# Performance work log

Hardware: AMD Instinct MI355X
Metric: run time of the kernel (lower is better)

The kernel has to match this reference:

```python
import jax, jax.numpy as jnp
import numpy as np
import math

B = 2048
NOSC = 64            # oscillators per modality
M = 3                # modalities (audio, text, vision) in sorted order
BDIM = 256           # binding_dim
DT = 0.01
NSTEPS = 10
DIMS = [512, 768, 1024]  # audio, text, vision
TWO_PI = 2.0 * math.pi


def setup_inputs() -> dict:
    key = jax.random.key(0)
    ks = iter(jax.random.split(key, 40))
    d = {}
    names = ['a', 't', 'v']
    for name, dim, x_key in zip(names, DIMS, ['x_audio', 'x_text', 'x_vision']):
        d[x_key] = jax.random.normal(next(ks), (B, dim), dtype=jnp.float32)
        s = 1.0 / math.sqrt(dim)
        d[f'Wf_{name}'] = jax.random.uniform(next(ks), (BDIM, dim), jnp.float32, -s, s)
        d[f'bf_{name}'] = jax.random.uniform(next(ks), (BDIM,), jnp.float32, -s, s)
        d[f'Wp_{name}'] = jax.random.uniform(next(ks), (NOSC, dim), jnp.float32, -s, s)
        d[f'bp_{name}'] = jax.random.uniform(next(ks), (NOSC,), jnp.float32, -s, s)
    # omegas: randn*0.1 + 1.0 + i*0.5 for i-th sorted modality
    for i, name in enumerate(names):
        d[f'omega_{name}'] = jax.random.normal(next(ks), (NOSC,), jnp.float32) * 0.1 + 1.0 + i * 0.5
    N = M * NOSC
    d['inter_coupling'] = jax.random.normal(next(ks), (N, N), jnp.float32) * 0.1
    s = 1.0 / math.sqrt(BDIM * M)
    d['W_fusion'] = jax.random.uniform(next(ks), (BDIM, BDIM * M), jnp.float32, -s, s)
    d['b_fusion'] = jax.random.uniform(next(ks), (BDIM,), jnp.float32, -s, s)
    return d


def reference(x_audio, x_text, x_vision,
              Wf_a, bf_a, Wp_a, bp_a,
              Wf_t, bf_t, Wp_t, bp_t,
              Wf_v, bf_v, Wp_v, bp_v,
              omega_a, omega_t, omega_v,
              inter_coupling, W_fusion, b_fusion):
    def enc(x, Wf, bf, Wp, bp):
        encoded = x @ Wf.T + bf                       # (B, BDIM)
        phases = (x @ Wp.T + bp) % TWO_PI             # (B, NOSC)
        return encoded, phases

    e_a, p_a = enc(x_audio, Wf_a, bf_a, Wp_a, bp_a)
    e_t, p_t = enc(x_text, Wf_t, bf_t, Wp_t, bp_t)
    e_v, p_v = enc(x_vision, Wf_v, bf_v, Wp_v, bp_v)

    phases = jnp.concatenate([p_a, p_t, p_v], axis=-1)        # (B, N)
    omega = jnp.concatenate([omega_a, omega_t, omega_v])      # (N,)
    K = (inter_coupling + inter_coupling.T) * 0.5             # (N, N)
    N = phases.shape[-1]

    def step(ph, _):
        diff = ph[:, :, None] - ph[:, None, :]                # (B, N, N)
        forces = jnp.einsum('ij,bij->bi', K, jnp.sin(diff)) / N
        ph = (ph + DT * (omega[None, :] + forces)) % TWO_PI
        return ph, None

    phases, _ = jax.lax.scan(step, phases, None, length=NSTEPS)

    pm = [phases[:, i * NOSC:(i + 1) * NOSC] for i in range(M)]  # per-modality

    # PLV between banks a,b: |mean_{i,j} exp(i(a_i - b_j))| = R_a * R_b where
    # R = |mean_k exp(i phi_k)| (resultant length), computed with real math.
    R = jnp.stack([jnp.sqrt(jnp.mean(jnp.cos(p), -1) ** 2 +
                            jnp.mean(jnp.sin(p), -1) ** 2) for p in pm])  # (M, B)
    bm = jnp.mean(R[:, None, :] * R[None, :, :], axis=-1)      # (M, M)
    binding_matrix = jnp.where(jnp.eye(M, dtype=bool), 1.0, bm)

    fused_parts = []
    for e, p in zip([e_a, e_t, e_v], pm):
        phase_mod = jnp.mean(jnp.cos(p), axis=-1, keepdims=True)  # (B, 1)
        fused_parts.append(e * (0.5 + 0.5 * phase_mod))
    fused = jnp.concatenate(fused_parts, axis=-1)              # (B, M*BDIM)
    bound = fused @ W_fusion.T + b_fusion                      # (B, BDIM)

    triu = jnp.triu(jnp.ones((M, M), dtype=bool), k=1)
    total = jnp.sum(jnp.where(triu, binding_matrix, 0.0)) / triu.sum()
    total_binding = jnp.full((bound.shape[0],), total)

    return bound, binding_matrix, phases, total_binding
```

## Files before the change

kernel.cpp:

```cpp
#include <hip/hip_runtime.h>
#include <math.h>

typedef short bf16x8 __attribute__((ext_vector_type(8)));
typedef short bf16x4 __attribute__((ext_vector_type(4)));
typedef float f32x4  __attribute__((ext_vector_type(4)));

#define INV_2PI  0.15915494309189535f
#define TWO_PI_F 6.283185307179586f
#define FSCALE   8.2893199e-06f

static __device__ inline short f2bf(float f) {
    union { float f; unsigned u; } v; v.f = f;
    unsigned r = (v.u + 0x7FFFu + ((v.u >> 16) & 1u)) >> 16;
    return (short)r;
}
static __device__ inline float bf2f(short h) {
    union { unsigned u; float f; } v; v.u = ((unsigned)(unsigned short)h) << 16;
    return v.f;
}

__global__ __launch_bounds__(256) void front_kernel(
    const float* __restrict__ xa, const float* __restrict__ xt, const float* __restrict__ xv,
    const float* __restrict__ Wpa, const float* __restrict__ Wpt, const float* __restrict__ Wpv,
    const float* __restrict__ IC,
    const float* __restrict__ oa, const float* __restrict__ ot, const float* __restrict__ ov,
    const float* __restrict__ bpa, const float* __restrict__ bpt, const float* __restrict__ bpv,
    float* __restrict__ partial, short* __restrict__ XB, short* __restrict__ Kp,
    float* __restrict__ om_eff, float* __restrict__ bp_all, float* __restrict__ bacc)
{
    __shared__ alignas(16) float As[16][72];
    __shared__ alignas(16) float Bs[16][72];
    int b = blockIdx.x;
    int t = threadIdx.x;

    if (b < 576) {
        int slot = b % 18, rb = b / 18;
        int z = slot < 4 ? 0 : (slot < 10 ? 1 : 2);
        int chunk = slot - (z == 0 ? 0 : (z == 1 ? 4 : 10));
        const float* A = z == 0 ? xa : (z == 1 ? xt : xv);
        const float* W = z == 0 ? Wpa : (z == 1 ? Wpt : Wpv);
        int K = z == 0 ? 512 : (z == 1 ? 768 : 1024);
        int kb = chunk * 128;
        int m0 = rb * 64;

        int tx = t & 15, ty = t >> 4;
        int row = t >> 2, c4 = t & 3;

        float acc[4][4] = {};
        float4 ar = *(const float4*)&A[(size_t)(m0 + row) * K + kb + c4 * 4];
        float4 br = *(const float4*)&W[(size_t)row * K + kb + c4 * 4];

        for (int k0 = 0; k0 < 128; k0 += 16) {
            if (k0) __syncthreads();
            As[c4 * 4 + 0][row] = ar.x;
            As[c4 * 4 + 1][row] = ar.y;
            As[c4 * 4 + 2][row] = ar.z;
            As[c4 * 4 + 3][row] = ar.w;
            Bs[c4 * 4 + 0][row] = br.x;
            Bs[c4 * 4 + 1][row] = br.y;
            Bs[c4 * 4 + 2][row] = br.z;
            Bs[c4 * 4 + 3][row] = br.w;
            __syncthreads();
            if (k0 + 16 < 128) {
                ar = *(const float4*)&A[(size_t)(m0 + row) * K + kb + k0 + 16 + c4 * 4];
                br = *(const float4*)&W[(size_t)row * K + kb + k0 + 16 + c4 * 4];
            }
#pragma unroll
            for (int kk = 0; kk < 16; ++kk) {
                float4 aq = *(const float4*)&As[kk][ty * 4];
                float4 bq = *(const float4*)&Bs[kk][tx * 4];
                float av[4] = {aq.x, aq.y, aq.z, aq.w};
                float bv[4] = {bq.x, bq.y, bq.z, bq.w};
#pragma unroll
                for (int i = 0; i < 4; ++i)
#pragma unroll
                    for (int j = 0; j < 4; ++j)
                        acc[i][j] += av[i] * bv[j];
            }
        }

        float* P = partial + (size_t)slot * 131072;
#pragma unroll
        for (int i = 0; i < 4; ++i) {
            float4 v = make_float4(acc[i][0], acc[i][1], acc[i][2], acc[i][3]);
            *(float4*)&P[(size_t)(m0 + ty * 4 + i) * 64 + tx * 4] = v;
        }
    } else if (b < 648) {
        for (int u = (b - 576) * 256 + t; u < 1179648; u += 72 * 256) {
            const float4* sp;
            if (u < 262144)      sp = (const float4*)xa + u;
            else if (u < 655360) sp = (const float4*)xt + (u - 262144);
            else                 sp = (const float4*)xv + (u - 655360);
            float4 v = *sp;
            bf16x4 h; h[0] = f2bf(v.x); h[1] = f2bf(v.y); h[2] = f2bf(v.z); h[3] = f2bf(v.w);
            *(bf16x4*)(XB + (size_t)u * 4) = h;
        }
    } else if (b < 680) {
        for (int idx = (b - 648) * 256 + t; idx < 36864; idx += 32 * 256) {
            int k = idx / 192, n = idx - k * 192;
            float v = 0.5f * (IC[k * 192 + n] + IC[n * 192 + k]);
            int nt = n >> 4, kc = k >> 5;
            int lane = ((k >> 3) & 3) * 16 + (n & 15);
            int j = k & 7;
            Kp[((nt * 6 + kc) * 64 + lane) * 8 + j] = f2bf(v);
        }
    } else {
        if (t < 192) {
            float w = t < 64 ? oa[t] : (t < 128 ? ot[t - 64] : ov[t - 128]);
            om_eff[t] = w * (0.01f * INV_2PI);
            float bb = t < 64 ? bpa[t] : (t < 128 ? bpt[t - 64] : bpv[t - 128]);
            bp_all[t] = bb;
        }
        if (t < 4) bacc[t] = 0.f;
    }
}

__global__ __launch_bounds__(256) void mid_kernel(
    const short* __restrict__ XB,
    const float* __restrict__ Wfa, const float* __restrict__ Wft, const float* __restrict__ Wfv,
    const float* __restrict__ ba, const float* __restrict__ bt, const float* __restrict__ bv,
    const float* __restrict__ partial, const float* __restrict__ bp_all,
    const short* __restrict__ Kp, const float* __restrict__ om_eff,
    short* __restrict__ e_bf16,
    float* __restrict__ phases_out, float* __restrict__ pm, float* __restrict__ bacc)
{
    __shared__ alignas(16) char smem[26816];
    int b = blockIdx.x;
    int t = threadIdx.x;
    int lane = t & 63, w = t >> 6;
    int q = lane >> 4, col = lane & 15;

    if (b < 384) {
        int z = b / 128, r = b % 128;
        int m0 = (r >> 2) * 64, n0 = (r & 3) * 64;
        const short* A    = XB + (z == 0 ? 0 : (z == 1 ? 1048576 : 2621440));
        const float* W    = z == 0 ? Wfa : (z == 1 ? Wft : Wfv);
        const float* bias = z == 0 ? ba : (z == 1 ? bt : bv);
        int K             = z == 0 ? 512 : (z == 1 ? 768 : 1024);

        short* As = (short*)smem;
        short* Bs = (short*)smem + 64 * 72;

        f32x4 acc[4];
#pragma unroll
        for (int f = 0; f < 4; ++f)
#pragma unroll
            for (int rr = 0; rr < 4; ++rr) acc[f][rr] = 0.f;

        bf16x8 av[2];
#pragma unroll
        for (int p = 0; p < 2; ++p) {
            int u = t + 256 * p;
            int arow = u >> 3, ac8 = u & 7;
            av[p] = *(const bf16x8*)&A[(size_t)(m0 + arow) * K + ac8 * 8];
        }
        float4 bv4[4];
#pragma unroll
        for (int p = 0; p < 4; ++p) {
            int u = t + 256 * p;
            int brow = u >> 4, bc4 = u & 15;
            bv4[p] = *(const float4*)&W[(size_t)(n0 + brow) * K + bc4 * 4];
        }

        for (int kb = 0; kb < K; kb += 64) {
            if (kb) __syncthreads();
#pragma unroll
            for (int p = 0; p < 2; ++p) {
                int u = t + 256 * p;
                int arow = u >> 3, ac8 = u & 7;
                *(bf16x8*)&As[arow * 72 + ac8 * 8] = av[p];
            }
#pragma unroll
            for (int p = 0; p < 4; ++p) {
                int u = t + 256 * p;
                int brow = u >> 4, bc4 = u & 15;
                bf16x4 h;
                h[0] = f2bf(bv4[p].x); h[1] = f2bf(bv4[p].y);
                h[2] = f2bf(bv4[p].z); h[3] = f2bf(bv4[p].w);
                *(bf16x4*)&Bs[brow * 72 + bc4 * 4] = h;
            }
            __syncthreads();
            if (kb + 64 < K) {
#pragma unroll
                for (int p = 0; p < 2; ++p) {
                    int u = t + 256 * p;
                    int arow = u >> 3, ac8 = u & 7;
                    av[p] = *(const bf16x8*)&A[(size_t)(m0 + arow) * K + kb + 64 + ac8 * 8];
                }
#pragma unroll
                for (int p = 0; p < 4; ++p) {
                    int u = t + 256 * p;
                    int brow = u >> 4, bc4 = u & 15;
                    bv4[p] = *(const float4*)&W[(size_t)(n0 + brow) * K + kb + 64 + bc4 * 4];
                }
            }

            bf16x8 bfr[2];
#pragma unroll
            for (int kc = 0; kc < 2; ++kc)
                bfr[kc] = *(const bf16x8*)&Bs[(w * 16 + col) * 72 + kc * 32 + q * 8];
#pragma unroll
            for (int f = 0; f < 4; ++f)
#pragma unroll
                for (int kc = 0; kc < 2; ++kc) {
                    bf16x8 af = *(const bf16x8*)&As[(f * 16 + col) * 72 + kc * 32 + q * 8];
                    acc[f] = __builtin_amdgcn_mfma_f32_16x16x32_bf16(af, bfr[kc], acc[f], 0, 0, 0);
                }
        }

        int n = n0 + w * 16 + col;
        float bn = bias[n];
#pragma unroll
        for (int f = 0; f < 4; ++f)
#pragma unroll
            for (int rr = 0; rr < 4; ++rr) {
                int m = m0 + f * 16 + q * 4 + rr;
                e_bf16[(size_t)m * 768 + z * 256 + n] = f2bf(acc[f][rr] + bn);
            }
    } else {
        short (*cs)[2][16][208] = (short (*)[2][16][208])smem;
        float (*Rl)[3] = (float (*)[3])(smem + 26624);

        int m0 = (b - 384) * 16;

        bf16x8 kb[3][6];
#pragma unroll
        for (int ntl = 0; ntl < 3; ++ntl)
#pragma unroll
            for (int kc = 0; kc < 6; ++kc) {
                int nt = w * 3 + ntl;
                kb[ntl][kc] = *(const bf16x8*)&Kp[((nt * 6 + kc) * 64 + lane) * 8];
            }

        float ph[3][4], om[3], c[3][4], s[3][4];
#pragma unroll
        for (int ntl = 0; ntl < 3; ++ntl) {
            int i = (w * 3 + ntl) * 16 + col;
            int z = i >> 6;
            int c0 = (z == 0) ? 0 : (z == 1 ? 4 : 10);
            int nch = (z == 0) ? 4 : (z == 1 ? 6 : 8);
            om[ntl] = om_eff[i];
#pragma unroll
            for (int r = 0; r < 4; ++r) {
                float raw = bp_all[i];
                size_t base = (size_t)c0 * 131072 + (size_t)(m0 + q * 4 + r) * 64 + (i & 63);
#pragma unroll
                for (int cc = 0; cc < 8; ++cc)
                    if (cc < nch) raw += partial[base + (size_t)cc * 131072];
                raw *= INV_2PI;
                ph[ntl][r] = raw - floorf(raw);
            }
        }

        for (int step = 0; step < 10; ++step) {
            int p = step & 1;
#pragma unroll
            for (int ntl = 0; ntl < 3; ++ntl) {
                int i = (w * 3 + ntl) * 16 + col;
#pragma unroll
                for (int r = 0; r < 4; ++r) {
                    c[ntl][r] = __builtin_amdgcn_cosf(ph[ntl][r]);
                    s[ntl][r] = __builtin_amdgcn_sinf(ph[ntl][r]);
                    cs[p][0][q * 4 + r][i] = f2bf(c[ntl][r]);
                    cs[p][1][q * 4 + r][i] = f2bf(s[ntl][r]);
                }
            }
            __syncthreads();

            f32x4 aC[3], aS[3];
#pragma unroll
            for (int ntl = 0; ntl < 3; ++ntl)
#pragma unroll
                for (int r = 0; r < 4; ++r) { aC[ntl][r] = 0.f; aS[ntl][r] = 0.f; }

#pragma unroll
            for (int kc = 0; kc < 6; ++kc) {
                bf16x8 ac  = *(const bf16x8*)&cs[p][0][col][kc * 32 + q * 8];
                bf16x8 as_ = *(const bf16x8*)&cs[p][1][col][kc * 32 + q * 8];
#pragma unroll
                for (int ntl = 0; ntl < 3; ++ntl) {
                    aC[ntl] = __builtin_amdgcn_mfma_f32_16x16x32_bf16(ac,  kb[ntl][kc], aC[ntl], 0, 0, 0);
                    aS[ntl] = __builtin_amdgcn_mfma_f32_16x16x32_bf16(as_, kb[ntl][kc], aS[ntl], 0, 0, 0);
                }
            }

#pragma unroll
            for (int ntl = 0; ntl < 3; ++ntl)
#pragma unroll
                for (int r = 0; r < 4; ++r) {
                    float f = (s[ntl][r] * aC[ntl][r] - c[ntl][r] * aS[ntl][r]) * FSCALE;
                    float pn = ph[ntl][r] + om[ntl] + f;
                    ph[ntl][r] = pn - floorf(pn);
                }
            if (step < 9) __syncthreads();
        }

        __syncthreads();
#pragma unroll
        for (int ntl = 0; ntl < 3; ++ntl) {
            int i = (w * 3 + ntl) * 16 + col;
#pragma unroll
            for (int r = 0; r < 4; ++r) {
                float cp = __builtin_amdgcn_cosf(ph[ntl][r]);
                float sp = __builtin_amdgcn_sinf(ph[ntl][r]);
                cs[0][0][q * 4 + r][i] = f2bf(cp);
                cs[0][1][q * 4 + r][i] = f2bf(sp);
                phases_out[(size_t)(m0 + q * 4 + r) * 192 + i] = ph[ntl][r] * TWO_PI_F;
            }
        }
        __syncthreads();

        if (t < 48) {
            int r = t & 15, mod = t >> 4;
            float sc = 0.f, ss = 0.f;
#pragma unroll
            for (int g = 0; g < 8; ++g) {
                bf16x8 vc = *(const bf16x8*)&cs[0][0][r][mod * 64 + g * 8];
                bf16x8 vs = *(const bf16x8*)&cs[0][1][r][mod * 64 + g * 8];
#pragma unroll
                for (int j = 0; j < 8; ++j) { sc += bf2f(vc[j]); ss += bf2f(vs[j]); }
            }
            sc *= (1.f / 64.f); ss *= (1.f / 64.f);
            pm[(size_t)(m0 + r) * 3 + mod] = 0.5f + 0.5f * sc;
            Rl[r][mod] = sqrtf(sc * sc + ss * ss);
        }
        __syncthreads();
        if (t < 3) {
            int a = (t == 2) ? 1 : 0;
            int bb = (t == 0) ? 1 : 2;
            float accp = 0.f;
            for (int r = 0; r < 16; ++r) accp += Rl[r][a] * Rl[r][bb];
            atomicAdd(&bacc[t], accp);
        }
    }
}

__global__ __launch_bounds__(256) void back_kernel(
    const short* __restrict__ e_bf16, const float* __restrict__ Wfu,
    const float* __restrict__ bias, const float* __restrict__ pm,
    const float* __restrict__ bacc,
    float* __restrict__ out_bound, float* __restrict__ out_bm, float* __restrict__ out_total)
{
    int m0 = blockIdx.x * 32, n0 = blockIdx.y * 64;
    int t = threadIdx.x;
    int lane = t & 63, w = t >> 6;
    int q = lane >> 4, col = lane & 15;

    __shared__ alignas(16) short As[32 * 72];
    __shared__ alignas(16) short Bs[64 * 72];

    int arow = t >> 3, ac8 = t & 7;

    f32x4 acc[2];
#pragma unroll
    for (int f = 0; f < 2; ++f)
#pragma unroll
        for (int r = 0; r < 4; ++r) acc[f][r] = 0.f;

    bf16x8 av = *(const bf16x8*)&e_bf16[(size_t)(m0 + arow) * 768 + ac8 * 8];
    float asc = pm[(size_t)(m0 + arow) * 3 + 0];
    float4 bv4[4];
#pragma unroll
    for (int p = 0; p < 4; ++p) {
        int u = t + 256 * p;
        int brow = u >> 4, bc4 = u & 15;
        bv4[p] = *(const float4*)&Wfu[(size_t)(n0 + brow) * 768 + bc4 * 4];
    }

    for (int kb = 0; kb < 768; kb += 64) {
        if (kb) __syncthreads();
        {
            bf16x8 h;
#pragma unroll
            for (int j = 0; j < 8; ++j) h[j] = f2bf(bf2f(av[j]) * asc);
            *(bf16x8*)&As[arow * 72 + ac8 * 8] = h;
        }
#pragma unroll
        for (int p = 0; p < 4; ++p) {
            int u = t + 256 * p;
            int brow = u >> 4, bc4 = u & 15;
            bf16x4 h;
            h[0] = f2bf(bv4[p].x); h[1] = f2bf(bv4[p].y);
            h[2] = f2bf(bv4[p].z); h[3] = f2bf(bv4[p].w);
            *(bf16x4*)&Bs[brow * 72 + bc4 * 4] = h;
        }
        __syncthreads();
        if (kb + 64 < 768) {
            int k = kb + 64;
            av = *(const bf16x8*)&e_bf16[(size_t)(m0 + arow) * 768 + k + ac8 * 8];
            asc = pm[(size_t)(m0 + arow) * 3 + (k >> 8)];
#pragma unroll
            for (int p = 0; p < 4; ++p) {
                int u = t + 256 * p;
                int brow = u >> 4, bc4 = u & 15;
                bv4[p] = *(const float4*)&Wfu[(size_t)(n0 + brow) * 768 + k + bc4 * 4];
            }
        }

        bf16x8 bfr[2];
#pragma unroll
        for (int kc = 0; kc < 2; ++kc)
            bfr[kc] = *(const bf16x8*)&Bs[(w * 16 + col) * 72 + kc * 32 + q * 8];
#pragma unroll
        for (int f = 0; f < 2; ++f)
#pragma unroll
            for (int kc = 0; kc < 2; ++kc) {
                bf16x8 af = *(const bf16x8*)&As[(f * 16 + col) * 72 + kc * 32 + q * 8];
                acc[f] = __builtin_amdgcn_mfma_f32_16x16x32_bf16(af, bfr[kc], acc[f], 0, 0, 0);
            }
    }

    int n = n0 + w * 16 + col;
    float bn = bias[n];
#pragma unroll
    for (int f = 0; f < 2; ++f)
#pragma unroll
        for (int r = 0; r < 4; ++r) {
            int m = m0 + f * 16 + q * 4 + r;
            out_bound[(size_t)m * 256 + n] = acc[f][r] + bn;
        }

    if (blockIdx.x == 0 && blockIdx.y == 0) {
        float p01 = bacc[0] * (1.f / 2048.f);
        float p02 = bacc[1] * (1.f / 2048.f);
        float p12 = bacc[2] * (1.f / 2048.f);
        float total = (p01 + p02 + p12) * (1.f / 3.f);
        if (t == 0) {
            out_bm[0] = 1.f; out_bm[1] = p01; out_bm[2] = p02;
            out_bm[3] = p01; out_bm[4] = 1.f; out_bm[5] = p12;
            out_bm[6] = p02; out_bm[7] = p12; out_bm[8] = 1.f;
        }
        for (int i = t; i < 2048; i += 256) out_total[i] = total;
    }
}

extern "C" void kernel_launch(void* const* d_in, const int* in_sizes, int n_in,
                              void* d_out, int out_size, void* d_ws, size_t ws_size,
                              hipStream_t stream)
{
    const float* x_a  = (const float*)d_in[0];
    const float* Wf_a = (const float*)d_in[1];
    const float* bf_a = (const float*)d_in[2];
    const float* Wp_a = (const float*)d_in[3];
    const float* bp_a = (const float*)d_in[4];
    const float* x_t  = (const float*)d_in[5];
    const float* Wf_t = (const float*)d_in[6];
    const float* bf_t = (const float*)d_in[7];
    const float* Wp_t = (const float*)d_in[8];
    const float* bp_t = (const float*)d_in[9];
    const float* x_v  = (const float*)d_in[10];
    const float* Wf_v = (const float*)d_in[11];
    const float* bf_v = (const float*)d_in[12];
    const float* Wp_v = (const float*)d_in[13];
    const float* bp_v = (const float*)d_in[14];
    const float* om_a = (const float*)d_in[15];
    const float* om_t = (const float*)d_in[16];
    const float* om_v = (const float*)d_in[17];
    const float* IC   = (const float*)d_in[18];
    const float* Wfu  = (const float*)d_in[19];
    const float* bfu  = (const float*)d_in[20];

    float* ws      = (float*)d_ws;
    float* omw     = ws;
    float* bpw     = ws + 256;
    float* pmv     = ws + 512;
    float* baccw   = ws + 6656;
    float* partial = ws + 6720;
    short* e_bf    = (short*)(ws + 2366016);
    short* XB      = (short*)(ws + 3152448);
    short* Kpck    = (short*)(ws + 5511744);

    float* out        = (float*)d_out;
    float* out_bound  = out;
    float* out_bm     = out + 524288;
    float* out_phases = out + 524297;
    float* out_total  = out + 917513;

    front_kernel<<<681, 256, 0, stream>>>(
        x_a, x_t, x_v, Wp_a, Wp_t, Wp_v,
        IC, om_a, om_t, om_v, bp_a, bp_t, bp_v,
        partial, XB, Kpck, omw, bpw, baccw);

    mid_kernel<<<512, 256, 0, stream>>>(
        XB, Wf_a, Wf_t, Wf_v, bf_a, bf_t, bf_v,
        partial, bpw, Kpck, omw,
        e_bf, out_phases, pmv, baccw);

    dim3 gF(64, 4);
    back_kernel<<<gF, 256, 0, stream>>>(e_bf, Wfu, bfu, pmv, baccw,
                                        out_bound, out_bm, out_total);
}
```

Before: 168.1 us.

## Fuse x-to-bf16 conversion into phase GEMM and pre-convert weights to bf16

The phase-projection GEMM blocks now write the bf16 copy of x as they load it, so the separate pass that re-read all inputs is gone. The freed blocks instead convert Wf_a/t/v and W_fusion to bf16 once into a workspace buffer. The mid and back GEMMs then load bf16 weights directly with 8-wide loads and skip the per-tile float-to-bf16 conversion and redundant fp32 weight reads. The cost is extra bf16 stores inside the GEMM loop and a larger workspace.

Result: faster. 155.4 us (-7.6%).

```diff
diff --git a/kernel.cpp b/kernel.cpp
--- a/kernel.cpp
+++ b/kernel.cpp
@@ -22,10 +22,13 @@
 __global__ __launch_bounds__(256) void front_kernel(
     const float* __restrict__ xa, const float* __restrict__ xt, const float* __restrict__ xv,
     const float* __restrict__ Wpa, const float* __restrict__ Wpt, const float* __restrict__ Wpv,
+    const float* __restrict__ Wfa, const float* __restrict__ Wft, const float* __restrict__ Wfv,
+    const float* __restrict__ Wfu,
     const float* __restrict__ IC,
     const float* __restrict__ oa, const float* __restrict__ ot, const float* __restrict__ ov,
     const float* __restrict__ bpa, const float* __restrict__ bpt, const float* __restrict__ bpv,
-    float* __restrict__ partial, short* __restrict__ XB, short* __restrict__ Kp,
+    float* __restrict__ partial, short* __restrict__ XB, short* __restrict__ WB,
+    short* __restrict__ Kp,
     float* __restrict__ om_eff, float* __restrict__ bp_all, float* __restrict__ bacc)
 {
     __shared__ alignas(16) float As[16][72];
@@ -39,6 +42,7 @@
         int chunk = slot - (z == 0 ? 0 : (z == 1 ? 4 : 10));
         const float* A = z == 0 ? xa : (z == 1 ? xt : xv);
         const float* W = z == 0 ? Wpa : (z == 1 ? Wpt : Wpv);
+        short* XBz = XB + (z == 0 ? 0 : (z == 1 ? 1048576 : 2621440));
         int K = z == 0 ? 512 : (z == 1 ? 768 : 1024);
         int kb = chunk * 128;
         int m0 = rb * 64;
@@ -60,6 +64,11 @@
             Bs[c4 * 4 + 1][row] = br.y;
             Bs[c4 * 4 + 2][row] = br.z;
             Bs[c4 * 4 + 3][row] = br.w;
+            {
+                bf16x4 h; h[0] = f2bf(ar.x); h[1] = f2bf(ar.y);
+                h[2] = f2bf(ar.z); h[3] = f2bf(ar.w);
+                *(bf16x4*)&XBz[(size_t)(m0 + row) * K + kb + k0 + c4 * 4] = h;
+            }
             __syncthreads();
             if (k0 + 16 < 128) {
                 ar = *(const float4*)&A[(size_t)(m0 + row) * K + kb + k0 + 16 + c4 * 4];
@@ -85,18 +94,19 @@
             float4 v = make_float4(acc[i][0], acc[i][1], acc[i][2], acc[i][3]);
             *(float4*)&P[(size_t)(m0 + ty * 4 + i) * 64 + tx * 4] = v;
         }
-    } else if (b < 648) {
-        for (int u = (b - 576) * 256 + t; u < 1179648; u += 72 * 256) {
+    } else if (b < 600) {
+        for (int u = (b - 576) * 256 + t; u < 196608; u += 24 * 256) {
             const float4* sp;
-            if (u < 262144)      sp = (const float4*)xa + u;
-            else if (u < 655360) sp = (const float4*)xt + (u - 262144);
-            else                 sp = (const float4*)xv + (u - 655360);
+            if (u < 32768)       sp = (const float4*)Wfa + u;
+            else if (u < 81920)  sp = (const float4*)Wft + (u - 32768);
+            else if (u < 147456) sp = (const float4*)Wfv + (u - 81920);
+            else                 sp = (const float4*)Wfu + (u - 147456);
             float4 v = *sp;
             bf16x4 h; h[0] = f2bf(v.x); h[1] = f2bf(v.y); h[2] = f2bf(v.z); h[3] = f2bf(v.w);
-            *(bf16x4*)(XB + (size_t)u * 4) = h;
-        }
-    } else if (b < 680) {
-        for (int idx = (b - 648) * 256 + t; idx < 36864; idx += 32 * 256) {
+            *(bf16x4*)(WB + (size_t)u * 4) = h;
+        }
+    } else if (b < 632) {
+        for (int idx = (b - 600) * 256 + t; idx < 36864; idx += 32 * 256) {
             int k = idx / 192, n = idx - k * 192;
             float v = 0.5f * (IC[k * 192 + n] + IC[n * 192 + k]);
             int nt = n >> 4, kc = k >> 5;
@@ -116,8 +126,7 @@
 }
 
 __global__ __launch_bounds__(256) void mid_kernel(
-    const short* __restrict__ XB,
-    const float* __restrict__ Wfa, const float* __restrict__ Wft, const float* __restrict__ Wfv,
+    const short* __restrict__ XB, const short* __restrict__ WB,
     const float* __restrict__ ba, const float* __restrict__ bt, const float* __restrict__ bv,
     const float* __restrict__ partial, const float* __restrict__ bp_all,
     const short* __restrict__ Kp, const float* __restrict__ om_eff,
@@ -134,64 +143,41 @@
         int z = b / 128, r = b % 128;
         int m0 = (r >> 2) * 64, n0 = (r & 3) * 64;
         const short* A    = XB + (z == 0 ? 0 : (z == 1 ? 1048576 : 2621440));
-        const float* W    = z == 0 ? Wfa : (z == 1 ? Wft : Wfv);
+        const short* W    = WB + (z == 0 ? 0 : (z == 1 ? 131072 : 327680));
         const float* bias = z == 0 ? ba : (z == 1 ? bt : bv);
         int K             = z == 0 ? 512 : (z == 1 ? 768 : 1024);
 
         short* As = (short*)smem;
         short* Bs = (short*)smem + 64 * 72;
 
+        int srow = t >> 3, sc8 = t & 7;
+
         f32x4 acc[4];
 #pragma unroll
         for (int f = 0; f < 4; ++f)
 #pragma unroll
             for (int rr = 0; rr < 4; ++rr) acc[f][rr] = 0.f;
 
-        bf16x8 av[2];
+        bf16x8 av[2], bv8[2];
 #pragma unroll
         for (int p = 0; p < 2; ++p) {
-            int u = t + 256 * p;
-            int arow = u >> 3, ac8 = u & 7;
-            av[p] = *(const bf16x8*)&A[(size_t)(m0 + arow) * K + ac8 * 8];
-        }
-        float4 bv4[4];
-#pragma unroll
-        for (int p = 0; p < 4; ++p) {
-            int u = t + 256 * p;
-            int brow = u >> 4, bc4 = u & 15;
-            bv4[p] = *(const float4*)&W[(size_t)(n0 + brow) * K + bc4 * 4];
+            av[p]  = *(const bf16x8*)&A[(size_t)(m0 + srow + 32 * p) * K + sc8 * 8];
+            bv8[p] = *(const bf16x8*)&W[(size_t)(n0 + srow + 32 * p) * K + sc8 * 8];
         }
 
         for (int kb = 0; kb < K; kb += 64) {
             if (kb) __syncthreads();
 #pragma unroll
             for (int p = 0; p < 2; ++p) {
-                int u = t + 256 * p;
-                int arow = u >> 3, ac8 = u & 7;
-                *(bf16x8*)&As[arow * 72 + ac8 * 8] = av[p];
-            }
-#pragma unroll
-            for (int p = 0; p < 4; ++p) {
-                int u = t + 256 * p;
-                int brow = u >> 4, bc4 = u & 15;
-                bf16x4 h;
-                h[0] = f2bf(bv4[p].x); h[1] = f2bf(bv4[p].y);
-                h[2] = f2bf(bv4[p].z); h[3] = f2bf(bv4[p].w);
-                *(bf16x4*)&Bs[brow * 72 + bc4 * 4] = h;
+                *(bf16x8*)&As[(srow + 32 * p) * 72 + sc8 * 8] = av[p];
+                *(bf16x8*)&Bs[(srow + 32 * p) * 72 + sc8 * 8] = bv8[p];
             }
             __syncthreads();
             if (kb + 64 < K) {
 #pragma unroll
                 for (int p = 0; p < 2; ++p) {
-                    int u = t + 256 * p;
-                    int arow = u >> 3, ac8 = u & 7;
-                    av[p] = *(const bf16x8*)&A[(size_t)(m0 + arow) * K + kb + 64 + ac8 * 8];
-                }
-#pragma unroll
-                for (int p = 0; p < 4; ++p) {
-                    int u = t + 256 * p;
-                    int brow = u >> 4, bc4 = u & 15;
-                    bv4[p] = *(const float4*)&W[(size_t)(n0 + brow) * K + kb + 64 + bc4 * 4];
+                    av[p]  = *(const bf16x8*)&A[(size_t)(m0 + srow + 32 * p) * K + kb + 64 + sc8 * 8];
+                    bv8[p] = *(const bf16x8*)&W[(size_t)(n0 + srow + 32 * p) * K + kb + 64 + sc8 * 8];
                 }
             }
 
@@ -336,11 +322,12 @@
 }
 
 __global__ __launch_bounds__(256) void back_kernel(
-    const short* __restrict__ e_bf16, const float* __restrict__ Wfu,
+    const short* __restrict__ e_bf16, const short* __restrict__ WB,
     const float* __restrict__ bias, const float* __restrict__ pm,
     const float* __restrict__ bacc,
     float* __restrict__ out_bound, float* __restrict__ out_bm, float* __restrict__ out_total)
 {
+    const short* Wfb = WB + 589824;
     int m0 = blockIdx.x * 32, n0 = blockIdx.y * 64;
     int t = threadIdx.x;
     int lane = t & 63, w = t >> 6;
@@ -349,7 +336,7 @@
     __shared__ alignas(16) short As[32 * 72];
     __shared__ alignas(16) short Bs[64 * 72];
 
-    int arow = t >> 3, ac8 = t & 7;
+    int srow = t >> 3, sc8 = t & 7;
 
     f32x4 acc[2];
 #pragma unroll
@@ -357,15 +344,12 @@
 #pragma unroll
         for (int r = 0; r < 4; ++r) acc[f][r] = 0.f;
 
-    bf16x8 av = *(const bf16x8*)&e_bf16[(size_t)(m0 + arow) * 768 + ac8 * 8];
-    float asc = pm[(size_t)(m0 + arow) * 3 + 0];
-    float4 bv4[4];
-#pragma unroll
-    for (int p = 0; p < 4; ++p) {
-        int u = t + 256 * p;
-        int brow = u >> 4, bc4 = u & 15;
-        bv4[p] = *(const float4*)&Wfu[(size_t)(n0 + brow) * 768 + bc4 * 4];
-    }
+    bf16x8 av = *(const bf16x8*)&e_bf16[(size_t)(m0 + srow) * 768 + sc8 * 8];
+    float asc = pm[(size_t)(m0 + srow) * 3 + 0];
+    bf16x8 bv8[2];
+#pragma unroll
+    for (int p = 0; p < 2; ++p)
+        bv8[p] = *(const bf16x8*)&Wfb[(size_t)(n0 + srow + 32 * p) * 768 + sc8 * 8];
 
     for (int kb = 0; kb < 768; kb += 64) {
         if (kb) __syncthreads();
@@ -373,28 +357,19 @@
             bf16x8 h;
 #pragma unroll
             for (int j = 0; j < 8; ++j) h[j] = f2bf(bf2f(av[j]) * asc);
-            *(bf16x8*)&As[arow * 72 + ac8 * 8] = h;
-        }
-#pragma unroll
-        for (int p = 0; p < 4; ++p) {
-            int u = t + 256 * p;
-            int brow = u >> 4, bc4 = u & 15;
-            bf16x4 h;
-            h[0] = f2bf(bv4[p].x); h[1] = f2bf(bv4[p].y);
-            h[2] = f2bf(bv4[p].z); h[3] = f2bf(bv4[p].w);
-            *(bf16x4*)&Bs[brow * 72 + bc4 * 4] = h;
-        }
+            *(bf16x8*)&As[srow * 72 + sc8 * 8] = h;
+        }
+#pragma unroll
+        for (int p = 0; p < 2; ++p)
+            *(bf16x8*)&Bs[(srow + 32 * p) * 72 + sc8 * 8] = bv8[p];
         __syncthreads();
         if (kb + 64 < 768) {
             int k = kb + 64;
-            av = *(const bf16x8*)&e_bf16[(size_t)(m0 + arow) * 768 + k + ac8 * 8];
-            asc = pm[(size_t)(m0 + arow) * 3 + (k >> 8)];
-#pragma unroll
-            for (int p = 0; p < 4; ++p) {
-                int u = t + 256 * p;
-                int brow = u >> 4, bc4 = u & 15;
-                bv4[p] = *(const float4*)&Wfu[(size_t)(n0 + brow) * 768 + k + bc4 * 4];
-            }
+            av = *(const bf16x8*)&e_bf16[(size_t)(m0 + srow) * 768 + k + sc8 * 8];
+            asc = pm[(size_t)(m0 + srow) * 3 + (k >> 8)];
+#pragma unroll
+            for (int p = 0; p < 2; ++p)
+                bv8[p] = *(const bf16x8*)&Wfb[(size_t)(n0 + srow + 32 * p) * 768 + k + sc8 * 8];
         }
 
         bf16x8 bfr[2];
@@ -469,6 +444,7 @@
     short* e_bf    = (short*)(ws + 2366016);
     short* XB      = (short*)(ws + 3152448);
     short* Kpck    = (short*)(ws + 5511744);
+    short* WB      = (short*)(ws + 5530176);
 
     float* out        = (float*)d_out;
     float* out_bound  = out;
@@ -476,17 +452,17 @@
     float* out_phases = out + 524297;
     float* out_total  = out + 917513;
 
-    front_kernel<<<681, 256, 0, stream>>>(
-        x_a, x_t, x_v, Wp_a, Wp_t, Wp_v,
+    front_kernel<<<633, 256, 0, stream>>>(
+        x_a, x_t, x_v, Wp_a, Wp_t, Wp_v, Wf_a, Wf_t, Wf_v, Wfu,
         IC, om_a, om_t, om_v, bp_a, bp_t, bp_v,
-        partial, XB, Kpck, omw, bpw, baccw);
+        partial, XB, WB, Kpck, omw, bpw, baccw);
 
     mid_kernel<<<512, 256, 0, stream>>>(
-        XB, Wf_a, Wf_t, Wf_v, bf_a, bf_t, bf_v,
+        XB, WB, bf_a, bf_t, bf_v,
         partial, bpw, Kpck, omw,
         e_bf, out_phases, pmv, baccw);
 
     dim3 gF(64, 4);
-    back_kernel<<<gF, 256, 0, stream>>>(e_bf, Wfu, bfu, pmv, baccw,
+    back_kernel<<<gF, 256, 0, stream>>>(e_bf, WB, bfu, pmv, baccw,
                                         out_bound, out_bm, out_total);
 }
```
